# Optimization experiments

Measured on AMD Instinct MI355X. Metric: run time of the kernel, lower is better.

Reference implementation:

```python
import jax, jax.numpy as jnp
import numpy as np

DK = 64
DROPOUT_P = 0.1


def setup_inputs() -> dict:
    key = jax.random.key(0)
    kq, kk, kv, km = jax.random.split(key, 4)
    B, S, D = 16, 2048, 64
    q = jax.random.normal(kq, (B, S, D), dtype=jnp.float32)
    k = jax.random.normal(kk, (B, S, D), dtype=jnp.float32)
    v = jax.random.normal(kv, (B, S, D), dtype=jnp.float32)
    attn_mask = jax.random.randint(km, (S, S), 0, 2, dtype=jnp.int32)
    return {"q": q, "k": k, "v": v, "attn_mask": attn_mask}


def reference(q, k, v, attn_mask):
    # q = q / sqrt(dk)
    qs = q * (1.0 / np.sqrt(DK)).astype(np.float32)
    # dots: [B, S_q, S_k]
    dots = jnp.einsum("bqd,bkd->bqk", qs, k)
    # mask: 0 -> -inf, 1 -> 0 (additive)
    add_mask = jnp.where(attn_mask == 0, -jnp.inf, 0.0).astype(dots.dtype)
    dots = dots + add_mask  # broadcast [S,S] over batch
    attn = jax.nn.softmax(dots, axis=-1)
    # inverted dropout, train mode, fixed key for determinism
    keep = jax.random.bernoulli(jax.random.key(42), 1.0 - DROPOUT_P, attn.shape)
    attn = jnp.where(keep, attn * (1.0 / (1.0 - DROPOUT_P)), 0.0)
    out = jnp.einsum("bqk,bkd->bqd", attn, v)
    return out
```

## Files before the change

kernel.cpp:

```cpp
#include <hip/hip_runtime.h>

#define BATCH 16
#define SEQ   2048
#define DIM   64
#define NTHREADS 256

typedef short bf16x8 __attribute__((ext_vector_type(8)));
typedef float f32x4 __attribute__((ext_vector_type(4)));

__device__ __forceinline__ int ldsoff(int row) {
  return row * 72 + 16 * (row >> 2);
}
#define LDS_SZ (64 * 72 + 16 * 16)

__device__ __forceinline__ unsigned tf_bits(unsigned f) {
  unsigned x0 = 0u;
  unsigned x1 = f;
  const unsigned ks1 = 42u;
  const unsigned ks2 = 0x1BD11BDAu ^ 42u;
  x1 += ks1;
#define TF_R(r) { x0 += x1; x1 = __builtin_amdgcn_alignbit(x1, x1, 32u - (r)); x1 ^= x0; }
  TF_R(13) TF_R(15) TF_R(26) TF_R(6)
  x0 += ks1; x1 += ks2 + 1u;
  TF_R(17) TF_R(29) TF_R(16) TF_R(24)
  x0 += ks2; x1 += 2u;
  TF_R(13) TF_R(15) TF_R(26) TF_R(6)
  x1 += ks1 + 3u;
  TF_R(17) TF_R(29) TF_R(16) TF_R(24)
  x0 += ks1; x1 += ks2 + 4u;
  TF_R(13) TF_R(15) TF_R(26) TF_R(6)
  x0 += ks2; x1 += 5u;
#undef TF_R
  return x0 ^ x1;
}
#define KEEP_THRESH 0xE6666600u

__device__ __forceinline__ unsigned pack_bf16x2(float lo, float hi) {
  const unsigned l = (__float_as_uint(lo) + 0x8000u) >> 16;
  const unsigned h = (__float_as_uint(hi) + 0x8000u) & 0xFFFF0000u;
  return h | l;
}
__device__ __forceinline__ unsigned pack_trunc(float lo, float hi) {
  return __builtin_amdgcn_perm(__float_as_uint(hi), __float_as_uint(lo), 0x07060302u);
}
__device__ __forceinline__ unsigned cvtpk(float lo, float hi) {
  unsigned r;
  asm("v_cvt_pk_bf16_f32 %0, %1, %2" : "=v"(r) : "v"(lo), "v"(hi));
  return r;
}

#define WS_KF 0
#define WS_VF 1048576
#define WS_MB 2097152

__global__ __launch_bounds__(NTHREADS)
void prep(const float* __restrict__ k, const float* __restrict__ v,
          const int* __restrict__ mask, unsigned* __restrict__ ws) {
  __shared__ float TS[64 * 68];
  const int t = threadIdx.x;
  const unsigned bx = blockIdx.x;

  if (bx < 1024) {
    const int x  = (int)bx & 7;
    const int j  = (int)bx >> 3;
    const int b  = 2 * x + (j & 1);
    const int j2 = j >> 1;
    const int kt = j2 & 31;
    const int kv = j2 >> 5;
    const float* src = (kv ? v : k) + ((size_t)b * SEQ + kt * 64) * DIM;

#pragma unroll
    for (int s = 0; s < 4; ++s) {
      const int row = s * 16 + (t >> 4);
      const int c4  = (t & 15) * 4;
      *(float4*)&TS[row * 68 + c4] = *(const float4*)(src + (size_t)row * DIM + c4);
    }
    __syncthreads();

    const int lane = t & 63, tx = lane & 15, quad = lane >> 4, sub = t >> 6;
    if (kv == 0) {
#pragma unroll
      for (int i = 0; i < 2; ++i) {
        const int combo = sub * 2 + i, nt = combo >> 1, ks = combo & 1;
        const float* rp = &TS[(4 * tx + nt) * 68 + ks * 32 + quad * 8];
        const float4 f0 = *(const float4*)rp;
        const float4 f1 = *(const float4*)(rp + 4);
        uint4 wout;
        wout.x = cvtpk(f0.x, f0.y); wout.y = cvtpk(f0.z, f0.w);
        wout.z = cvtpk(f1.x, f1.y); wout.w = cvtpk(f1.z, f1.w);
        const unsigned e = ((((unsigned)b * 32 + kt) * 4 + nt) * 2 + ks) * 64 + lane;
        *(uint4*)(ws + WS_KF + (size_t)e * 4) = wout;
      }
    } else {
#pragma unroll
      for (int i = 0; i < 2; ++i) {
        const int combo = sub * 2 + i, nt = combo >> 1, ks = combo & 1;
        const float* cp = &TS[(ks * 32 + quad * 8) * 68 + nt * 16 + tx];
        uint4 wout;
        wout.x = cvtpk(cp[0 * 68], cp[1 * 68]);
        wout.y = cvtpk(cp[2 * 68], cp[3 * 68]);
        wout.z = cvtpk(cp[4 * 68], cp[5 * 68]);
        wout.w = cvtpk(cp[6 * 68], cp[7 * 68]);
        const unsigned e = ((((unsigned)b * 32 + kt) * 4 + nt) * 2 + ks) * 64 + lane;
        *(uint4*)(ws + WS_VF + (size_t)e * 4) = wout;
      }
    }
    return;
  }

  const unsigned pid = (bx - 1024u) * NTHREADS + (unsigned)t;
  const unsigned C4 = pid & 511u, R4 = pid >> 9;
  unsigned m16 = 0u;
#pragma unroll
  for (int rr = 0; rr < 4; ++rr) {
    const int4 mv = *(const int4*)(mask + (size_t)(4 * R4 + rr) * SEQ + 4 * C4);
    m16 |= (mv.x ? 1u : 0u) << (rr * 4 + 0);
    m16 |= (mv.y ? 1u : 0u) << (rr * 4 + 1);
    m16 |= (mv.z ? 1u : 0u) << (rr * 4 + 2);
    m16 |= (mv.w ? 1u : 0u) << (rr * 4 + 3);
  }
  ((unsigned short*)(ws + WS_MB))[pid] = (unsigned short)m16;
}

__global__ __launch_bounds__(NTHREADS, 4)
void attn_fwd(const float* __restrict__ q, const unsigned* __restrict__ ws,
              float* __restrict__ out) {
  __shared__ __align__(16) unsigned short PS[LDS_SZ];

  const int t    = threadIdx.x;
  const int w    = t >> 6;
  const int lane = t & 63;
  const int tx   = lane & 15;
  const int quad = lane >> 4;
  const int rh   = w & 1;
  const int kh   = w >> 1;

  const int x  = (int)blockIdx.x & 7;
  const int j  = (int)blockIdx.x >> 3;
  const int bb = 2 * x + (j & 1);
  const int qb = (j >> 1) * 32;
  const int qw = qb + 16 * rh;
  const int kt0 = kh * 16;

  const float qscale = 0.125f * 1.44269504088896340736f;

  bf16x8 aq[2];
  {
    const float* qr = q + ((size_t)bb * SEQ + qw + tx) * DIM + quad * 8;
#pragma unroll
    for (int ks = 0; ks < 2; ++ks) {
      const float4 f0 = *(const float4*)(qr + ks * 32);
      const float4 f1 = *(const float4*)(qr + ks * 32 + 4);
      union { unsigned u[4]; bf16x8 v; } a;
      a.u[0] = pack_bf16x2(f0.x * qscale, f0.y * qscale);
      a.u[1] = pack_bf16x2(f0.z * qscale, f0.w * qscale);
      a.u[2] = pack_bf16x2(f1.x * qscale, f1.y * qscale);
      a.u[3] = pack_bf16x2(f1.z * qscale, f1.w * qscale);
      aq[ks] = a.v;
    }
  }

  float lrun[4] = {0.f, 0.f, 0.f, 0.f};
  f32x4 oacc[4];
#pragma unroll
  for (int nt = 0; nt < 4; ++nt) oacc[nt] = (f32x4){0.f, 0.f, 0.f, 0.f};

  const unsigned* kfb = ws + WS_KF + (size_t)(bb * 32) * 2048 + (size_t)lane * 4;
  const unsigned* vfb = ws + WS_VF + (size_t)(bb * 32) * 2048 + (size_t)lane * 4;
  const unsigned short* maskp = (const unsigned short*)(ws + WS_MB)
      + ((size_t)((qw >> 2) + quad)) * 512 + tx;
  const unsigned fbase0 = (unsigned)(bb * SEQ + qw + quad * 4) * (unsigned)SEQ
                          + (unsigned)(4 * tx);

  bf16x8 vf[4][2];

#define RNG_PWRITE(kt_, qk_, mw_)                                              \
  {                                                                            \
    const unsigned fb = fbase0 + (unsigned)((kt_) * 64);                       \
    _Pragma("unroll")                                                          \
    for (int reg = 0; reg < 4; ++reg) {                                        \
      const unsigned mnib = (mw_) >> (reg * 4);                                \
      float pd[4];                                                             \
      float ls = 0.0f;                                                         \
      _Pragma("unroll")                                                        \
      for (int nt = 0; nt < 4; ++nt) {                                         \
        const float s = (mnib & (1u << nt)) ? qk_[nt][reg] : -1e30f;           \
        const float e = __builtin_amdgcn_exp2f(s);                             \
        ls += e;                                                               \
        const unsigned bits = tf_bits(fb + (unsigned)(reg * SEQ) + (unsigned)nt); \
        pd[nt] = (bits < KEEP_THRESH) ? e : 0.0f;                              \
      }                                                                        \
      lrun[reg] += ls;                                                         \
      uint2 pw;                                                                \
      pw.x = pack_trunc(pd[0], pd[1]);                                         \
      pw.y = pack_trunc(pd[2], pd[3]);                                         \
      *(uint2*)&PS[ldsoff(16 * w + quad * 4 + reg) + 4 * tx] = pw;             \
    }                                                                          \
  }

#define LOAD_KF(kt_)                                                           \
    const unsigned* kfp = kfb + (size_t)(kt_) * 2048;                          \
    bf16x8 kf[4][2];                                                           \
    _Pragma("unroll")                                                          \
    for (int nt = 0; nt < 4; ++nt)                                             \
      _Pragma("unroll")                                                        \
      for (int ks = 0; ks < 2; ++ks)                                           \
        kf[nt][ks] = *(const bf16x8*)(kfp + (nt * 2 + ks) * 256);

#define PV_STEP                                                                \
    _Pragma("unroll")                                                          \
    for (int ks = 0; ks < 2; ++ks) {                                           \
      const bf16x8 ap = *(const bf16x8*)&PS[ldsoff(16 * w + tx) + ks * 32 + quad * 8]; \
      _Pragma("unroll")                                                        \
      for (int nt = 0; nt < 4; ++nt)                                           \
        oacc[nt] = __builtin_amdgcn_mfma_f32_16x16x32_bf16(ap, vf[nt][ks],     \
                                                           oacc[nt], 0, 0, 0); \
    }

#define LOAD_VF(kt_)                                                           \
    const unsigned* vfp = vfb + (size_t)(kt_) * 2048;                          \
    _Pragma("unroll")                                                          \
    for (int nt = 0; nt < 4; ++nt)                                             \
      _Pragma("unroll")                                                        \
      for (int ks = 0; ks < 2; ++ks)                                           \
        vf[nt][ks] = *(const bf16x8*)(vfp + (nt * 2 + ks) * 256);

#define QK_STEP(qk_)                                                           \
    f32x4 qk_[4];                                                              \
    _Pragma("unroll")                                                          \
    for (int nt = 0; nt < 4; ++nt) {                                           \
      f32x4 c = (f32x4){0.f, 0.f, 0.f, 0.f};                                   \
      _Pragma("unroll")                                                        \
      for (int ks = 0; ks < 2; ++ks)                                           \
        c = __builtin_amdgcn_mfma_f32_16x16x32_bf16(aq[ks], kf[nt][ks], c, 0, 0, 0); \
      qk_[nt] = c;                                                             \
    }

  {
    LOAD_KF(kt0)
    LOAD_VF(kt0)
    const unsigned mwv = maskp[kt0 * 16];
    QK_STEP(qk)
    RNG_PWRITE(kt0, qk, mwv)
  }
#pragma unroll 1
  for (int kt = kt0 + 1; kt < kt0 + 16; ++kt) {
    LOAD_KF(kt)
    const unsigned mwv = maskp[kt * 16];
    PV_STEP
    LOAD_VF(kt)
    QK_STEP(qk)
    RNG_PWRITE(kt, qk, mwv)
  }
  PV_STEP

  float lsum[4];
#pragma unroll
  for (int reg = 0; reg < 4; ++reg) {
    float ls = lrun[reg];
    ls += __shfl_xor(ls, 1);
    ls += __shfl_xor(ls, 2);
    ls += __shfl_xor(ls, 4);
    ls += __shfl_xor(ls, 8);
    lsum[reg] = ls;
  }

  __syncthreads();
  float* MB = (float*)PS;
  float* ML = MB + 2048;
  if (kh == 1) {
#pragma unroll
    for (int nt = 0; nt < 4; ++nt)
#pragma unroll
      for (int reg = 0; reg < 4; ++reg)
        MB[(16 * rh + quad * 4 + reg) * 64 + nt * 16 + tx] = oacc[nt][reg];
    if (tx == 0) {
#pragma unroll
      for (int reg = 0; reg < 4; ++reg)
        ML[16 * rh + quad * 4 + reg] = lsum[reg];
    }
  }
  __syncthreads();
  if (kh == 0) {
    float linv[4];
#pragma unroll
    for (int reg = 0; reg < 4; ++reg)
      linv[reg] = (1.0f / 0.9f) / (lsum[reg] + ML[16 * rh + quad * 4 + reg]);
    float* ob = out + ((size_t)bb * SEQ + qw) * DIM;
#pragma unroll
    for (int nt = 0; nt < 4; ++nt)
#pragma unroll
      for (int reg = 0; reg < 4; ++reg)
        ob[(size_t)(quad * 4 + reg) * DIM + nt * 16 + tx] =
            (oacc[nt][reg] + MB[(16 * rh + quad * 4 + reg) * 64 + nt * 16 + tx])
            * linv[reg];
  }
}

extern "C" void kernel_launch(void* const* d_in, const int* in_sizes, int n_in,
                              void* d_out, int out_size, void* d_ws, size_t ws_size,
                              hipStream_t stream) {
  const float* q = (const float*)d_in[0];
  const float* k = (const float*)d_in[1];
  const float* v = (const float*)d_in[2];
  const int* mask = (const int*)d_in[3];
  float* out = (float*)d_out;
  unsigned* ws = (unsigned*)d_ws;

  hipLaunchKernelGGL(prep, dim3(2048), dim3(NTHREADS), 0, stream,
                     k, v, mask, ws);
  hipLaunchKernelGGL(attn_fwd, dim3(1024), dim3(NTHREADS), 0, stream,
                     q, ws, out);
}
```

Before: 220.3 us.

## Fuse prep and attention kernels with a grid-wide atomic barrier

Merges the K/V bf16 conversion and mask bit-packing prep kernel into the attention kernel. Each of the 1024 blocks does its share of prep, then all blocks meet at a global atomic-counter spin barrier before the attention phase. This removes one kernel launch and the gap between kernels. In exchange it adds a memset launch and a spin wait. It relies on all 1024 blocks being co-resident (256 CUs x 4 blocks), otherwise it deadlocks or times out after the bounded spin.

```diff
diff --git a/kernel.cpp b/kernel.cpp
--- a/kernel.cpp
+++ b/kernel.cpp
@@ -49,96 +49,102 @@
   return r;
 }
 
-#define WS_KF 0
-#define WS_VF 1048576
-#define WS_MB 2097152
-
-__global__ __launch_bounds__(NTHREADS)
-void prep(const float* __restrict__ k, const float* __restrict__ v,
-          const int* __restrict__ mask, unsigned* __restrict__ ws) {
-  __shared__ float TS[64 * 68];
-  const int t = threadIdx.x;
-  const unsigned bx = blockIdx.x;
-
-  if (bx < 1024) {
-    const int x  = (int)bx & 7;
-    const int j  = (int)bx >> 3;
-    const int b  = 2 * x + (j & 1);
-    const int j2 = j >> 1;
-    const int kt = j2 & 31;
-    const int kv = j2 >> 5;
-    const float* src = (kv ? v : k) + ((size_t)b * SEQ + kt * 64) * DIM;
-
+#define WS_KF  0
+#define WS_VF  1048576
+#define WS_MB  2097152
+#define WS_CNT 2228224
+
+__global__ __launch_bounds__(NTHREADS, 4)
+void attn_all(const float* __restrict__ q, const float* __restrict__ k,
+              const float* __restrict__ v, const int* __restrict__ mask,
+              float* __restrict__ out, unsigned* __restrict__ ws) {
+  __shared__ __align__(16) union {
+    float TS[64 * 68];
+    unsigned short PS[LDS_SZ];
+  } sh;
+
+  const int t    = threadIdx.x;
+  const int w    = t >> 6;
+  const int lane = t & 63;
+  const int tx   = lane & 15;
+  const int quad = lane >> 4;
+
+  const int x  = (int)blockIdx.x & 7;
+  const int j  = (int)blockIdx.x >> 3;
+  const int bb = 2 * x + (j & 1);
+  const int u  = j >> 1;
+
+  {
+    const int kt = u & 31, kv = u >> 5;
+    const float* src = (kv ? v : k) + ((size_t)bb * SEQ + kt * 64) * DIM;
 #pragma unroll
     for (int s = 0; s < 4; ++s) {
       const int row = s * 16 + (t >> 4);
       const int c4  = (t & 15) * 4;
-      *(float4*)&TS[row * 68 + c4] = *(const float4*)(src + (size_t)row * DIM + c4);
+      *(float4*)&sh.TS[row * 68 + c4] = *(const float4*)(src + (size_t)row * DIM + c4);
     }
     __syncthreads();
-
-    const int lane = t & 63, tx = lane & 15, quad = lane >> 4, sub = t >> 6;
+    const int sub = t >> 6;
     if (kv == 0) {
 #pragma unroll
       for (int i = 0; i < 2; ++i) {
         const int combo = sub * 2 + i, nt = combo >> 1, ks = combo & 1;
-        const float* rp = &TS[(4 * tx + nt) * 68 + ks * 32 + quad * 8];
+        const float* rp = &sh.TS[(4 * tx + nt) * 68 + ks * 32 + quad * 8];
         const float4 f0 = *(const float4*)rp;
         const float4 f1 = *(const float4*)(rp + 4);
         uint4 wout;
         wout.x = cvtpk(f0.x, f0.y); wout.y = cvtpk(f0.z, f0.w);
         wout.z = cvtpk(f1.x, f1.y); wout.w = cvtpk(f1.z, f1.w);
-        const unsigned e = ((((unsigned)b * 32 + kt) * 4 + nt) * 2 + ks) * 64 + lane;
+        const unsigned e = ((((unsigned)bb * 32 + kt) * 4 + nt) * 2 + ks) * 64 + lane;
         *(uint4*)(ws + WS_KF + (size_t)e * 4) = wout;
       }
     } else {
 #pragma unroll
       for (int i = 0; i < 2; ++i) {
         const int combo = sub * 2 + i, nt = combo >> 1, ks = combo & 1;
-        const float* cp = &TS[(ks * 32 + quad * 8) * 68 + nt * 16 + tx];
+        const float* cp = &sh.TS[(ks * 32 + quad * 8) * 68 + nt * 16 + tx];
         uint4 wout;
         wout.x = cvtpk(cp[0 * 68], cp[1 * 68]);
         wout.y = cvtpk(cp[2 * 68], cp[3 * 68]);
         wout.z = cvtpk(cp[4 * 68], cp[5 * 68]);
         wout.w = cvtpk(cp[6 * 68], cp[7 * 68]);
-        const unsigned e = ((((unsigned)b * 32 + kt) * 4 + nt) * 2 + ks) * 64 + lane;
+        const unsigned e = ((((unsigned)bb * 32 + kt) * 4 + nt) * 2 + ks) * 64 + lane;
         *(uint4*)(ws + WS_VF + (size_t)e * 4) = wout;
       }
     }
-    return;
-  }
-
-  const unsigned pid = (bx - 1024u) * NTHREADS + (unsigned)t;
-  const unsigned C4 = pid & 511u, R4 = pid >> 9;
-  unsigned m16 = 0u;
-#pragma unroll
-  for (int rr = 0; rr < 4; ++rr) {
-    const int4 mv = *(const int4*)(mask + (size_t)(4 * R4 + rr) * SEQ + 4 * C4);
-    m16 |= (mv.x ? 1u : 0u) << (rr * 4 + 0);
-    m16 |= (mv.y ? 1u : 0u) << (rr * 4 + 1);
-    m16 |= (mv.z ? 1u : 0u) << (rr * 4 + 2);
-    m16 |= (mv.w ? 1u : 0u) << (rr * 4 + 3);
-  }
-  ((unsigned short*)(ws + WS_MB))[pid] = (unsigned short)m16;
-}
-
-__global__ __launch_bounds__(NTHREADS, 4)
-void attn_fwd(const float* __restrict__ q, const unsigned* __restrict__ ws,
-              float* __restrict__ out) {
-  __shared__ __align__(16) unsigned short PS[LDS_SZ];
-
-  const int t    = threadIdx.x;
-  const int w    = t >> 6;
-  const int lane = t & 63;
-  const int tx   = lane & 15;
-  const int quad = lane >> 4;
-  const int rh   = w & 1;
-  const int kh   = w >> 1;
-
-  const int x  = (int)blockIdx.x & 7;
-  const int j  = (int)blockIdx.x >> 3;
-  const int bb = 2 * x + (j & 1);
-  const int qb = (j >> 1) * 32;
+  }
+
+  {
+    const unsigned pid = (unsigned)blockIdx.x * NTHREADS + (unsigned)t;
+    const unsigned C4 = pid & 511u, R4 = pid >> 9;
+    unsigned m16 = 0u;
+#pragma unroll
+    for (int rr = 0; rr < 4; ++rr) {
+      const int4 mv = *(const int4*)(mask + (size_t)(4 * R4 + rr) * SEQ + 4 * C4);
+      m16 |= (mv.x ? 1u : 0u) << (rr * 4 + 0);
+      m16 |= (mv.y ? 1u : 0u) << (rr * 4 + 1);
+      m16 |= (mv.z ? 1u : 0u) << (rr * 4 + 2);
+      m16 |= (mv.w ? 1u : 0u) << (rr * 4 + 3);
+    }
+    ((unsigned short*)(ws + WS_MB))[pid] = (unsigned short)m16;
+  }
+
+  __threadfence();
+  __syncthreads();
+  if (t == 0) {
+    atomicAdd(ws + WS_CNT, 1u);
+    for (int it = 0; it < (1 << 20); ++it) {
+      if (__hip_atomic_load(ws + WS_CNT, __ATOMIC_ACQUIRE,
+                            __HIP_MEMORY_SCOPE_AGENT) >= 1024u) break;
+      __builtin_amdgcn_s_sleep(8);
+    }
+  }
+  __syncthreads();
+  __threadfence();
+
+  const int rh = w & 1;
+  const int kh = w >> 1;
+  const int qb = u * 32;
   const int qw = qb + 16 * rh;
   const int kt0 = kh * 16;
 
@@ -151,11 +157,11 @@
     for (int ks = 0; ks < 2; ++ks) {
       const float4 f0 = *(const float4*)(qr + ks * 32);
       const float4 f1 = *(const float4*)(qr + ks * 32 + 4);
-      union { unsigned u[4]; bf16x8 v; } a;
-      a.u[0] = pack_bf16x2(f0.x * qscale, f0.y * qscale);
-      a.u[1] = pack_bf16x2(f0.z * qscale, f0.w * qscale);
-      a.u[2] = pack_bf16x2(f1.x * qscale, f1.y * qscale);
-      a.u[3] = pack_bf16x2(f1.z * qscale, f1.w * qscale);
+      union { unsigned uu[4]; bf16x8 v; } a;
+      a.uu[0] = pack_bf16x2(f0.x * qscale, f0.y * qscale);
+      a.uu[1] = pack_bf16x2(f0.z * qscale, f0.w * qscale);
+      a.uu[2] = pack_bf16x2(f1.x * qscale, f1.y * qscale);
+      a.uu[3] = pack_bf16x2(f1.z * qscale, f1.w * qscale);
       aq[ks] = a.v;
     }
   }
@@ -194,7 +200,7 @@
       uint2 pw;                                                                \
       pw.x = pack_trunc(pd[0], pd[1]);                                         \
       pw.y = pack_trunc(pd[2], pd[3]);                                         \
-      *(uint2*)&PS[ldsoff(16 * w + quad * 4 + reg) + 4 * tx] = pw;             \
+      *(uint2*)&sh.PS[ldsoff(16 * w + quad * 4 + reg) + 4 * tx] = pw;          \
     }                                                                          \
   }
 
@@ -210,7 +216,7 @@
 #define PV_STEP                                                                \
     _Pragma("unroll")                                                          \
     for (int ks = 0; ks < 2; ++ks) {                                           \
-      const bf16x8 ap = *(const bf16x8*)&PS[ldsoff(16 * w + tx) + ks * 32 + quad * 8]; \
+      const bf16x8 ap = *(const bf16x8*)&sh.PS[ldsoff(16 * w + tx) + ks * 32 + quad * 8]; \
       _Pragma("unroll")                                                        \
       for (int nt = 0; nt < 4; ++nt)                                           \
         oacc[nt] = __builtin_amdgcn_mfma_f32_16x16x32_bf16(ap, vf[nt][ks],     \
@@ -266,7 +272,7 @@
   }
 
   __syncthreads();
-  float* MB = (float*)PS;
+  float* MB = (float*)sh.PS;
   float* ML = MB + 2048;
   if (kh == 1) {
 #pragma unroll
@@ -307,8 +313,7 @@
   float* out = (float*)d_out;
   unsigned* ws = (unsigned*)d_ws;
 
-  hipLaunchKernelGGL(prep, dim3(2048), dim3(NTHREADS), 0, stream,
-                     k, v, mask, ws);
-  hipLaunchKernelGGL(attn_fwd, dim3(1024), dim3(NTHREADS), 0, stream,
-                     q, ws, out);
-}
+  hipMemsetAsync((char*)d_ws + (size_t)WS_CNT * 4, 0, 4, stream);
+  hipLaunchKernelGGL(attn_all, dim3(1024), dim3(NTHREADS), 0, stream,
+                     q, k, v, mask, out, ws);
+}
```

After: 473.7 us. 115% more time.
